# Kernel tuning notes

Measured on AMD Instinct MI355X. Metric: run time of the kernel, lower is better.

The kernel has to match this reference:

```python
import jax, jax.numpy as jnp
import numpy as np

B, T, E, H = 8, 1024, 1024, 16
D = E // H  # head_dim = 64
MAX_OFFSET = 0.5


def setup_inputs() -> dict:
    key = jax.random.key(0)
    ks = jax.random.split(key, 12)
    s = 0.02
    return {
        "query": jax.random.normal(ks[0], (B, T, E), jnp.float32),
        "key_": jax.random.normal(ks[1], (B, T, E), jnp.float32),
        "value": jax.random.normal(ks[2], (B, T, E), jnp.float32),
        "Wq": jax.random.normal(ks[3], (E, E), jnp.float32) * s,
        "bq": jnp.zeros((E,), jnp.float32),
        "Wk": jax.random.normal(ks[4], (E, E), jnp.float32) * s,
        "bk": jnp.zeros((E,), jnp.float32),
        "Wv": jax.random.normal(ks[5], (E, E), jnp.float32) * s,
        "bv": jnp.zeros((E,), jnp.float32),
        "Wo": jax.random.normal(ks[6], (E, E), jnp.float32) * s,
        "bo": jnp.zeros((E,), jnp.float32),
        "bias_table": jax.random.normal(ks[7], (2 * T - 1, H), jnp.float32) * s,
        "offset": jax.random.normal(ks[8], (1,), jnp.float32) * 0.1,
    }


def _temporal_bias(bias_table, offset):
    # relative position index: [T, T] in [0, 2T-2]
    coords = jnp.arange(T)
    rel = (coords[:, None] - coords[None, :]) + (T - 1)
    bounded = jnp.tanh(offset) * MAX_OFFSET  # scalar (shape (1,))
    adj = jnp.clip(rel.astype(jnp.float32) + bounded, 0.0, 2.0 * T - 2.0)
    lo = jnp.floor(adj).astype(jnp.int32)
    hi = jnp.ceil(adj).astype(jnp.int32)
    w = adj - lo.astype(jnp.float32)  # [T, T]
    lo_val = bias_table[lo]  # [T, T, H]
    hi_val = bias_table[hi]  # [T, T, H]
    bias = lo_val * (1.0 - w[..., None]) + hi_val * w[..., None]
    # -> [1, H, T, T]
    return jnp.transpose(bias, (2, 0, 1))[None]


def reference(query, key_, value, Wq, bq, Wk, bk, Wv, bv, Wo, bo, bias_table, offset):
    scale = D ** -0.5
    # torch Linear: x @ W.T + b
    q = (jnp.einsum('bte,fe->btf', query, Wq) + bq).reshape(B, T, H, D).transpose(0, 2, 1, 3)
    k = (jnp.einsum('bte,fe->btf', key_, Wk) + bk).reshape(B, T, H, D).transpose(0, 2, 1, 3)
    v = (jnp.einsum('bte,fe->btf', value, Wv) + bv).reshape(B, T, H, D).transpose(0, 2, 1, 3)
    scores = jnp.einsum('bhqd,bhkd->bhqk', q, k) * scale  # [B, H, T, T]
    scores = scores + _temporal_bias(bias_table, offset)
    attn = jax.nn.softmax(scores, axis=-1)
    out = jnp.einsum('bhqk,bhkd->bhqd', attn, v)  # [B, H, T, D]
    out = out.transpose(0, 2, 1, 3).reshape(B, T, E)
    return jnp.einsum('bte,fe->btf', out, Wo) + bo
```

## Files before the change

### kernel.cpp

```cpp
#include <hip/hip_runtime.h>
#include <hip/hip_bf16.h>
#include <stdint.h>

#define B_ 8
#define T_ 1024
#define E_ 1024
#define H_ 16
#define D_ 64
#define NREL 2047

using bf16 = __hip_bfloat16;
typedef __attribute__((ext_vector_type(8))) short bhalf8;
typedef __attribute__((ext_vector_type(4))) float f32x4;

typedef __attribute__((address_space(3))) uint32_t lds32_t;
typedef const __attribute__((address_space(1))) uint32_t glb32_t;
__device__ __forceinline__ void gld_lds16(const bf16* g, bf16* l) {
  __builtin_amdgcn_global_load_lds((glb32_t*)(const void*)g, (lds32_t*)(void*)l, 16, 0, 0);
}

__global__ __launch_bounds__(256) void cvt_f32_bf16(const float* __restrict__ s,
                                                    bf16* __restrict__ d, int n) {
  const int i = (blockIdx.x * 256 + threadIdx.x) * 8;
  if (i >= n) return;
  const float4 a = *(const float4*)(s + i);
  const float4 b = *(const float4*)(s + i + 4);
  bf16 t[8];
  t[0] = __float2bfloat16(a.x); t[1] = __float2bfloat16(a.y);
  t[2] = __float2bfloat16(a.z); t[3] = __float2bfloat16(a.w);
  t[4] = __float2bfloat16(b.x); t[5] = __float2bfloat16(b.y);
  t[6] = __float2bfloat16(b.z); t[7] = __float2bfloat16(b.w);
  *(bhalf8*)(d + i) = *(const bhalf8*)t;
}

__global__ void bias_pre(const float* __restrict__ table, const float* __restrict__ offset,
                         float* __restrict__ db) {
  const int idx = blockIdx.x * 256 + threadIdx.x;
  if (idx >= NREL * H_) return;
  const int r = idx >> 4;
  const int h = idx & 15;
  const float bounded = tanhf(offset[0]) * 0.5f;
  float adj = (float)r + bounded;
  adj = fminf(fmaxf(adj, 0.f), 2046.f);
  const int lo = (int)floorf(adj);
  const int hi = (int)ceilf(adj);
  const float wgt = adj - (float)lo;
  const float v = table[lo * H_ + h] * (1.f - wgt) + table[hi * H_ + h] * wgt;
  db[h * NREL + r] = v * 1.4426950408889634f;
}

__global__ __launch_bounds__(256, 3) void gemm_qkv(const float* __restrict__ Xq,
                                                   const float* __restrict__ Xk,
                                                   const float* __restrict__ Xv,
                                                   const bf16* __restrict__ Wc,
                                                   const float* __restrict__ bqp,
                                                   const float* __restrict__ bkp,
                                                   const float* __restrict__ bvp,
                                                   bf16* __restrict__ dst) {
  __shared__ bf16 As[128 * 32];
  __shared__ bf16 Bs[128 * 32];
  const int tid = threadIdx.x;
  const int lane = tid & 63;
  const int w = tid >> 6;
  const int quad = lane >> 4;
  const int l15 = lane & 15;
  const int m0 = blockIdx.x * 128;
  const int n0 = blockIdx.y * 128;
  const int z = blockIdx.z;
  const float* A = (z == 0) ? Xq : ((z == 1) ? Xk : Xv);
  const float* bias = (z == 0) ? bqp : ((z == 1) ? bkp : bvp);
  const bf16* W = Wc + (size_t)z * E_ * E_;
  bf16* out = dst + (size_t)z * B_ * T_ * D_ * H_;
  const int wm = (w >> 1) * 64;
  const int wn = (w & 1) * 64;

  const f32x4 zero4 = {0.f, 0.f, 0.f, 0.f};
  f32x4 acc[4][4];
#pragma unroll
  for (int i = 0; i < 4; ++i)
#pragma unroll
    for (int j = 0; j < 4; ++j) acc[i][j] = zero4;

  const int srow = w * 32 + (lane >> 2);
  const int scol = (lane & 3) * 8;
  const float* Ag = A + (size_t)(m0 + srow) * E_ + scol;
  const bf16* Wg = W + (size_t)(n0 + srow) * E_ + scol;
  bf16* As0 = As + w * 1024 + lane * 8;
  bf16* Bs0 = Bs + w * 1024 + lane * 8;

  float4 p0 = *(const float4*)(Ag);
  float4 p1 = *(const float4*)(Ag + 4);
  float4 p2 = *(const float4*)(Ag + (size_t)16 * E_);
  float4 p3 = *(const float4*)(Ag + (size_t)16 * E_ + 4);

  for (int kt = 0; kt < 32; ++kt) {
    __syncthreads();
    const int kc = kt * 32;
    gld_lds16(Wg + kc, Bs0);
    gld_lds16(Wg + (size_t)16 * E_ + kc, Bs0 + 512);
    const float4 a0 = p0, a1 = p1, a2 = p2, a3 = p3;
    if (kt < 31) {
      const int kc2 = kc + 32;
      p0 = *(const float4*)(Ag + kc2);
      p1 = *(const float4*)(Ag + kc2 + 4);
      p2 = *(const float4*)(Ag + (size_t)16 * E_ + kc2);
      p3 = *(const float4*)(Ag + (size_t)16 * E_ + kc2 + 4);
    }
    bf16 t[8];
    t[0] = __float2bfloat16(a0.x); t[1] = __float2bfloat16(a0.y);
    t[2] = __float2bfloat16(a0.z); t[3] = __float2bfloat16(a0.w);
    t[4] = __float2bfloat16(a1.x); t[5] = __float2bfloat16(a1.y);
    t[6] = __float2bfloat16(a1.z); t[7] = __float2bfloat16(a1.w);
    *(bhalf8*)As0 = *(const bhalf8*)t;
    t[0] = __float2bfloat16(a2.x); t[1] = __float2bfloat16(a2.y);
    t[2] = __float2bfloat16(a2.z); t[3] = __float2bfloat16(a2.w);
    t[4] = __float2bfloat16(a3.x); t[5] = __float2bfloat16(a3.y);
    t[6] = __float2bfloat16(a3.z); t[7] = __float2bfloat16(a3.w);
    *(bhalf8*)(As0 + 512) = *(const bhalf8*)t;
    __syncthreads();

    bhalf8 af[4], bfr[4];
#pragma unroll
    for (int t2 = 0; t2 < 4; ++t2) {
      af[t2] = *(const bhalf8*)(As + (wm + t2 * 16 + l15) * 32 + quad * 8);
      bfr[t2] = *(const bhalf8*)(Bs + (wn + t2 * 16 + l15) * 32 + quad * 8);
    }
#pragma unroll
    for (int mt = 0; mt < 4; ++mt)
#pragma unroll
      for (int nt = 0; nt < 4; ++nt)
        acc[mt][nt] = __builtin_amdgcn_mfma_f32_16x16x32_bf16(af[mt], bfr[nt], acc[mt][nt], 0, 0, 0);
  }

#pragma unroll
  for (int mt = 0; mt < 4; ++mt) {
#pragma unroll
    for (int nt = 0; nt < 4; ++nt) {
      const int n = n0 + wn + nt * 16 + l15;
      const float bv = bias[n];
#pragma unroll
      for (int r = 0; r < 4; ++r) {
        const int m = m0 + wm + mt * 16 + quad * 4 + r;
        const float v = acc[mt][nt][r] + bv;
        const int bb = m >> 10, tq = m & 1023, hh = n >> 6, d = n & 63;
        out[(((size_t)bb * H_ + hh) * T_ + tq) * D_ + d] = __float2bfloat16(v);
      }
    }
  }
}

template <int SCATTER, int F32OUT>
__global__ __launch_bounds__(256) void gemm_bt(const bf16* __restrict__ A,
                                               const bf16* __restrict__ W,
                                               const float* __restrict__ bias,
                                               void* __restrict__ dst_) {
  __shared__ bf16 As[128 * 32];
  __shared__ bf16 Bs[128 * 32];
  const int tid = threadIdx.x;
  const int lane = tid & 63;
  const int w = tid >> 6;
  const int quad = lane >> 4;
  const int l15 = lane & 15;
  const int m0 = blockIdx.x * 128;
  const int n0 = blockIdx.y * 128;
  const int wm = (w >> 1) * 64;
  const int wn = (w & 1) * 64;

  const f32x4 zero4 = {0.f, 0.f, 0.f, 0.f};
  f32x4 acc[4][4];
#pragma unroll
  for (int i = 0; i < 4; ++i)
#pragma unroll
    for (int j = 0; j < 4; ++j) acc[i][j] = zero4;

  const int srow0 = w * 32 + (lane >> 2);
  const int scol = (lane & 3) * 8;
  const bf16* Ag = A + (size_t)(m0 + srow0) * E_ + scol;
  const bf16* Wg = W + (size_t)(n0 + srow0) * E_ + scol;
  bf16* As0 = As + w * 1024 + lane * 8;
  bf16* Bs0 = Bs + w * 1024 + lane * 8;

  for (int kt = 0; kt < 32; ++kt) {
    __syncthreads();
    const int kc = kt * 32;
    gld_lds16(Ag + kc, As0);
    gld_lds16(Ag + (size_t)16 * E_ + kc, As0 + 512);
    gld_lds16(Wg + kc, Bs0);
    gld_lds16(Wg + (size_t)16 * E_ + kc, Bs0 + 512);
    __syncthreads();

    bhalf8 af[4], bfr[4];
#pragma unroll
    for (int t = 0; t < 4; ++t) {
      af[t] = *(const bhalf8*)(As + (wm + t * 16 + l15) * 32 + quad * 8);
      bfr[t] = *(const bhalf8*)(Bs + (wn + t * 16 + l15) * 32 + quad * 8);
    }
#pragma unroll
    for (int mt = 0; mt < 4; ++mt)
#pragma unroll
      for (int nt = 0; nt < 4; ++nt)
        acc[mt][nt] = __builtin_amdgcn_mfma_f32_16x16x32_bf16(af[mt], bfr[nt], acc[mt][nt], 0, 0, 0);
  }

#pragma unroll
  for (int mt = 0; mt < 4; ++mt) {
#pragma unroll
    for (int nt = 0; nt < 4; ++nt) {
      const int n = n0 + wn + nt * 16 + l15;
      const float bv = bias[n];
#pragma unroll
      for (int r = 0; r < 4; ++r) {
        const int m = m0 + wm + mt * 16 + quad * 4 + r;
        const float v = acc[mt][nt][r] + bv;
        if (SCATTER) {
          const int bb = m >> 10, t = m & 1023, hh = n >> 6, d = n & 63;
          ((bf16*)dst_)[(((size_t)bb * H_ + hh) * T_ + t) * D_ + d] = __float2bfloat16(v);
        } else if (F32OUT) {
          ((float*)dst_)[(size_t)m * E_ + n] = v;
        } else {
          ((bf16*)dst_)[(size_t)m * E_ + n] = __float2bfloat16(v);
        }
      }
    }
  }
}

__device__ __forceinline__ int ps_off(int row, int colbyte) {
  return row * 128 + (colbyte ^ ((row & 7) << 4));
}

__global__ __launch_bounds__(256, 4) void attn_kernel(const bf16* __restrict__ Q,
                                                      const bf16* __restrict__ K,
                                                      const bf16* __restrict__ V,
                                                      const float* __restrict__ db,
                                                      bf16* __restrict__ xout) {
  const int tid = threadIdx.x;
  const int lane = tid & 63;
  const int w = tid >> 6;
  const int quad = lane >> 4;
  const int l15 = lane & 15;
  const int bh = blockIdx.x;
  const int h = bh & 15;
  const int b = bh >> 4;
  const int q0 = blockIdx.y * 128;

  __shared__ bf16 Vt[64][72];
  __shared__ __align__(16) bf16 Ps[4][32 * 64];
  __shared__ float dbs[1152];

  const size_t base = (size_t)bh * T_ * D_;
  const bf16* Qp = Q + base;
  const bf16* Kp = K + base;
  const bf16* Vp = V + base;
  const float* dbh = db + h * NREL;

  for (int t = tid; t < 1151; t += 256) dbs[t] = dbh[q0 + t];

  const int qw = q0 + w * 32;
  bhalf8 aq[2][2];
#pragma unroll
  for (int mt = 0; mt < 2; ++mt)
#pragma unroll
    for (int ks = 0; ks < 2; ++ks)
      aq[mt][ks] = *(const bhalf8*)(Qp + (size_t)(qw + mt * 16 + l15) * D_ + ks * 32 + quad * 8);

  const f32x4 zero4 = {0.f, 0.f, 0.f, 0.f};
  f32x4 o[2][4];
#pragma unroll
  for (int mt = 0; mt < 2; ++mt)
#pragma unroll
    for (int nt = 0; nt < 4; ++nt) o[mt][nt] = zero4;
  float mrow[2] = {-1e30f, -1e30f};
  float lrow[2] = {0.f, 0.f};

  const int vrow0 = tid >> 3;
  const int vc8 = (tid & 7) * 8;
  bhalf8 vreg[2];
  vreg[0] = *(const bhalf8*)(Vp + (size_t)vrow0 * D_ + vc8);
  vreg[1] = *(const bhalf8*)(Vp + (size_t)(vrow0 + 32) * D_ + vc8);

  char* const psw = (char*)&Ps[w][0];

  for (int it = 0; it < 16; ++it) {
    const int kb = it * 64;
    bhalf8 bk[4][2];
#pragma unroll
    for (int nt = 0; nt < 4; ++nt) {
      const bf16* kr = Kp + (size_t)(kb + nt * 16 + l15) * D_ + quad * 8;
      bk[nt][0] = *(const bhalf8*)kr;
      bk[nt][1] = *(const bhalf8*)(kr + 32);
    }

    __syncthreads();
#pragma unroll
    for (int s = 0; s < 2; ++s) {
      const int row = vrow0 + s * 32;
      const bf16* vp = (const bf16*)&vreg[s];
      const int kvp = (row + vc8) & 63;
#pragma unroll
      for (int j = 0; j < 8; ++j) Vt[vc8 + j][kvp] = vp[j];
    }
    __syncthreads();
    if (it < 15) {
      const int kb2 = kb + 64;
      vreg[0] = *(const bhalf8*)(Vp + (size_t)(kb2 + vrow0) * D_ + vc8);
      vreg[1] = *(const bhalf8*)(Vp + (size_t)(kb2 + vrow0 + 32) * D_ + vc8);
    }

    f32x4 s4[2][4];
    __builtin_amdgcn_s_setprio(1);
#pragma unroll
    for (int nt = 0; nt < 4; ++nt) {
#pragma unroll
      for (int mt = 0; mt < 2; ++mt) {
        f32x4 a = zero4;
        a = __builtin_amdgcn_mfma_f32_16x16x32_bf16(bk[nt][0], aq[mt][0], a, 0, 0, 0);
        a = __builtin_amdgcn_mfma_f32_16x16x32_bf16(bk[nt][1], aq[mt][1], a, 0, 0, 0);
        s4[mt][nt] = a;
      }
    }
    __builtin_amdgcn_s_setprio(0);

#pragma unroll
    for (int mt = 0; mt < 2; ++mt) {
      const int ib = w * 32 + mt * 16 + l15 + 1023 - kb;
      float mnt[4];
#pragma unroll
      for (int nt = 0; nt < 4; ++nt) {
#pragma unroll
        for (int r = 0; r < 4; ++r) {
          const float sv = s4[mt][nt][r] * 0.18033688011112042f + dbs[ib - nt * 16 - quad * 4 - r];
          s4[mt][nt][r] = sv;
        }
        mnt[nt] = fmaxf(fmaxf(s4[mt][nt][0], s4[mt][nt][1]),
                        fmaxf(s4[mt][nt][2], s4[mt][nt][3]));
      }
      float tmx = fmaxf(fmaxf(mnt[0], mnt[1]), fmaxf(mnt[2], mnt[3]));
      tmx = fmaxf(tmx, __shfl_xor(tmx, 16, 64));
      tmx = fmaxf(tmx, __shfl_xor(tmx, 32, 64));
      if (!__all(tmx - mrow[mt] <= 11.0f)) {
        const float mnew = fmaxf(mrow[mt], tmx);
        const float alpha = __builtin_amdgcn_exp2f(mrow[mt] - mnew);
        mrow[mt] = mnew;
        lrow[mt] *= alpha;
#pragma unroll
        for (int nt = 0; nt < 4; ++nt) o[mt][nt] *= alpha;
      }
      const float mcur = mrow[mt];
      float psum[4];
#pragma unroll
      for (int nt = 0; nt < 4; ++nt) {
        float p0 = __builtin_amdgcn_exp2f(s4[mt][nt][0] - mcur);
        float p1 = __builtin_amdgcn_exp2f(s4[mt][nt][1] - mcur);
        float p2 = __builtin_amdgcn_exp2f(s4[mt][nt][2] - mcur);
        float p3 = __builtin_amdgcn_exp2f(s4[mt][nt][3] - mcur);
        s4[mt][nt][0] = p0; s4[mt][nt][1] = p1;
        s4[mt][nt][2] = p2; s4[mt][nt][3] = p3;
        psum[nt] = (p0 + p1) + (p2 + p3);
      }
      float sum = (psum[0] + psum[1]) + (psum[2] + psum[3]);
      sum += __shfl_xor(sum, 16, 64);
      sum += __shfl_xor(sum, 32, 64);
      lrow[mt] += sum;

#pragma unroll
      for (int nt = 0; nt < 4; ++nt) {
        alignas(8) bf16 t4[4];
#pragma unroll
        for (int r = 0; r < 4; ++r) t4[r] = __float2bfloat16(s4[mt][nt][r]);
        *(uint2*)(psw + ps_off(mt * 16 + l15, nt * 32 + quad * 8)) = *(const uint2*)t4;
      }
    }

    bhalf8 pb[2][2];
#pragma unroll
    for (int mt = 0; mt < 2; ++mt)
#pragma unroll
      for (int ks = 0; ks < 2; ++ks)
        pb[mt][ks] = *(const bhalf8*)(psw + ps_off(mt * 16 + l15, ks * 64 + quad * 16));
    const int rot = (l15 >> 3);
    __builtin_amdgcn_s_setprio(1);
#pragma unroll
    for (int nt = 0; nt < 4; ++nt) {
      const int drow = nt * 16 + l15;
#pragma unroll
      for (int ks = 0; ks < 2; ++ks) {
        const int gp = (4 * ks + quad + 2 * nt + rot) & 7;
        const bhalf8 vb = *(const bhalf8*)&Vt[drow][gp * 8];
#pragma unroll
        for (int mt = 0; mt < 2; ++mt)
          o[mt][nt] = __builtin_amdgcn_mfma_f32_16x16x32_bf16(vb, pb[mt][ks], o[mt][nt], 0, 0, 0);
      }
    }
    __builtin_amdgcn_s_setprio(0);
  }

#pragma unroll
  for (int mt = 0; mt < 2; ++mt) {
    const float inv = 1.f / lrow[mt];
#pragma unroll
    for (int nt = 0; nt < 4; ++nt) {
      alignas(8) bf16 t4[4];
#pragma unroll
      for (int r = 0; r < 4; ++r) t4[r] = __float2bfloat16(o[mt][nt][r] * inv);
      *(uint2*)(psw + ps_off(mt * 16 + l15, nt * 32 + quad * 8)) = *(const uint2*)t4;
    }
  }
#pragma unroll
  for (int t = 0; t < 4; ++t) {
    const int idx = t * 64 + lane;
    const int row = idx >> 3;
    const int c = idx & 7;
    const bhalf8 val = *(const bhalf8*)(psw + ps_off(row, c * 16));
    *(bhalf8*)&xout[((size_t)b * T_ + qw + row) * E_ + h * D_ + c * 8] = val;
  }
}

extern "C" void kernel_launch(void* const* d_in, const int* in_sizes, int n_in,
                              void* d_out, int out_size, void* d_ws, size_t ws_size,
                              hipStream_t stream) {
  const float* query = (const float*)d_in[0];
  const float* key_  = (const float*)d_in[1];
  const float* value = (const float*)d_in[2];
  const float* Wq = (const float*)d_in[3];
  const float* bq = (const float*)d_in[4];
  const float* Wk = (const float*)d_in[5];
  const float* bk = (const float*)d_in[6];
  const float* Wv = (const float*)d_in[7];
  const float* bv = (const float*)d_in[8];
  const float* Wo = (const float*)d_in[9];
  const float* bo = (const float*)d_in[10];
  const float* table = (const float*)d_in[11];
  const float* offset = (const float*)d_in[12];
  float* out = (float*)d_out;

  char* ws = (char*)d_ws;
  const size_t ME = (size_t)B_ * T_ * E_;
  const size_t EE = (size_t)E_ * E_;
  float* db = (float*)ws;
  bf16* wc  = (bf16*)(ws + 131072);
  bf16* qb  = wc + 4 * EE;
  bf16* kb  = qb + ME;
  bf16* vb2 = kb + ME;
  bf16* x2  = vb2 + ME;

  dim3 bb(256, 1, 1);
  const int gEE = (int)(EE / 8 / 256);

  bias_pre<<<dim3(128), bb, 0, stream>>>(table, offset, db);

  cvt_f32_bf16<<<dim3(gEE), bb, 0, stream>>>(Wq, wc + 0 * EE, (int)EE);
  cvt_f32_bf16<<<dim3(gEE), bb, 0, stream>>>(Wk, wc + 1 * EE, (int)EE);
  cvt_f32_bf16<<<dim3(gEE), bb, 0, stream>>>(Wv, wc + 2 * EE, (int)EE);
  cvt_f32_bf16<<<dim3(gEE), bb, 0, stream>>>(Wo, wc + 3 * EE, (int)EE);

  gemm_qkv<<<dim3(64, 8, 3), bb, 0, stream>>>(query, key_, value, wc, bq, bk, bv, qb);

  attn_kernel<<<dim3(128, 8, 1), bb, 0, stream>>>(qb, kb, vb2, db, x2);

  gemm_bt<0, 1><<<dim3(64, 8, 1), bb, 0, stream>>>(x2, wc + 3 * EE, bo, out);
}
```

Measured before the change: 354.8 us.

## Double-buffer LDS tiles in projection GEMMs and merge weight conversion launches

Both the QKV projection GEMM and the output GEMM now use two LDS buffers per operand. The next K-tile is loaded, and for QKV the fp32 activations are converted into the alternate buffer, while MFMAs run on the current one. This cuts the loop to one barrier per iteration instead of two and hides global-load latency. The four weight-conversion launches are also merged into one 2D-grid launch. The cost is doubled LDS per block (32 KB), which may lower occupancy, notably against the launch bound of 3 blocks requested for gemm_qkv.

```diff
diff --git a/kernel.cpp b/kernel.cpp
--- a/kernel.cpp
+++ b/kernel.cpp
@@ -19,18 +19,26 @@
   __builtin_amdgcn_global_load_lds((glb32_t*)(const void*)g, (lds32_t*)(void*)l, 16, 0, 0);
 }
 
-__global__ __launch_bounds__(256) void cvt_f32_bf16(const float* __restrict__ s,
-                                                    bf16* __restrict__ d, int n) {
-  const int i = (blockIdx.x * 256 + threadIdx.x) * 8;
-  if (i >= n) return;
-  const float4 a = *(const float4*)(s + i);
-  const float4 b = *(const float4*)(s + i + 4);
+__device__ __forceinline__ bhalf8 cvt8(const float4 a, const float4 b) {
   bf16 t[8];
   t[0] = __float2bfloat16(a.x); t[1] = __float2bfloat16(a.y);
   t[2] = __float2bfloat16(a.z); t[3] = __float2bfloat16(a.w);
   t[4] = __float2bfloat16(b.x); t[5] = __float2bfloat16(b.y);
   t[6] = __float2bfloat16(b.z); t[7] = __float2bfloat16(b.w);
-  *(bhalf8*)(d + i) = *(const bhalf8*)t;
+  return *(const bhalf8*)t;
+}
+
+__global__ __launch_bounds__(256) void cvt_w4(const float* __restrict__ Wq,
+                                              const float* __restrict__ Wk,
+                                              const float* __restrict__ Wv,
+                                              const float* __restrict__ Wo,
+                                              bf16* __restrict__ d) {
+  const int z = blockIdx.y;
+  const float* s = (z == 0) ? Wq : (z == 1) ? Wk : (z == 2) ? Wv : Wo;
+  const int i = (blockIdx.x * 256 + threadIdx.x) * 8;
+  const float4 a = *(const float4*)(s + i);
+  const float4 b = *(const float4*)(s + i + 4);
+  *(bhalf8*)(d + (size_t)z * E_ * E_ + i) = cvt8(a, b);
 }
 
 __global__ void bias_pre(const float* __restrict__ table, const float* __restrict__ offset,
@@ -57,8 +65,8 @@
                                                    const float* __restrict__ bkp,
                                                    const float* __restrict__ bvp,
                                                    bf16* __restrict__ dst) {
-  __shared__ bf16 As[128 * 32];
-  __shared__ bf16 Bs[128 * 32];
+  __shared__ bf16 As[2 * 128 * 32];
+  __shared__ bf16 Bs[2 * 128 * 32];
   const int tid = threadIdx.x;
   const int lane = tid & 63;
   const int w = tid >> 6;
@@ -85,51 +93,51 @@
   const int scol = (lane & 3) * 8;
   const float* Ag = A + (size_t)(m0 + srow) * E_ + scol;
   const bf16* Wg = W + (size_t)(n0 + srow) * E_ + scol;
-  bf16* As0 = As + w * 1024 + lane * 8;
-  bf16* Bs0 = Bs + w * 1024 + lane * 8;
+  const int sidx = w * 1024 + lane * 8;
 
   float4 p0 = *(const float4*)(Ag);
   float4 p1 = *(const float4*)(Ag + 4);
   float4 p2 = *(const float4*)(Ag + (size_t)16 * E_);
   float4 p3 = *(const float4*)(Ag + (size_t)16 * E_ + 4);
+  *(bhalf8*)(As + sidx) = cvt8(p0, p1);
+  *(bhalf8*)(As + sidx + 512) = cvt8(p2, p3);
+  gld_lds16(Wg, Bs + sidx);
+  gld_lds16(Wg + (size_t)16 * E_, Bs + sidx + 512);
+  p0 = *(const float4*)(Ag + 32);
+  p1 = *(const float4*)(Ag + 36);
+  p2 = *(const float4*)(Ag + (size_t)16 * E_ + 32);
+  p3 = *(const float4*)(Ag + (size_t)16 * E_ + 36);
+  __syncthreads();
 
   for (int kt = 0; kt < 32; ++kt) {
-    __syncthreads();
-    const int kc = kt * 32;
-    gld_lds16(Wg + kc, Bs0);
-    gld_lds16(Wg + (size_t)16 * E_ + kc, Bs0 + 512);
-    const float4 a0 = p0, a1 = p1, a2 = p2, a3 = p3;
+    const int cur = (kt & 1) * 4096;
+    bhalf8 af[4], bfr[4];
+#pragma unroll
+    for (int t2 = 0; t2 < 4; ++t2) {
+      af[t2] = *(const bhalf8*)(As + cur + (wm + t2 * 16 + l15) * 32 + quad * 8);
+      bfr[t2] = *(const bhalf8*)(Bs + cur + (wn + t2 * 16 + l15) * 32 + quad * 8);
+    }
     if (kt < 31) {
-      const int kc2 = kc + 32;
-      p0 = *(const float4*)(Ag + kc2);
-      p1 = *(const float4*)(Ag + kc2 + 4);
-      p2 = *(const float4*)(Ag + (size_t)16 * E_ + kc2);
-      p3 = *(const float4*)(Ag + (size_t)16 * E_ + kc2 + 4);
-    }
-    bf16 t[8];
-    t[0] = __float2bfloat16(a0.x); t[1] = __float2bfloat16(a0.y);
-    t[2] = __float2bfloat16(a0.z); t[3] = __float2bfloat16(a0.w);
-    t[4] = __float2bfloat16(a1.x); t[5] = __float2bfloat16(a1.y);
-    t[6] = __float2bfloat16(a1.z); t[7] = __float2bfloat16(a1.w);
-    *(bhalf8*)As0 = *(const bhalf8*)t;
-    t[0] = __float2bfloat16(a2.x); t[1] = __float2bfloat16(a2.y);
-    t[2] = __float2bfloat16(a2.z); t[3] = __float2bfloat16(a2.w);
-    t[4] = __float2bfloat16(a3.x); t[5] = __float2bfloat16(a3.y);
-    t[6] = __float2bfloat16(a3.z); t[7] = __float2bfloat16(a3.w);
-    *(bhalf8*)(As0 + 512) = *(const bhalf8*)t;
-    __syncthreads();
-
-    bhalf8 af[4], bfr[4];
-#pragma unroll
-    for (int t2 = 0; t2 < 4; ++t2) {
-      af[t2] = *(const bhalf8*)(As + (wm + t2 * 16 + l15) * 32 + quad * 8);
-      bfr[t2] = *(const bhalf8*)(Bs + (wn + t2 * 16 + l15) * 32 + quad * 8);
+      const int nxt = 4096 - cur;
+      const int kc = (kt + 1) * 32;
+      gld_lds16(Wg + kc, Bs + nxt + sidx);
+      gld_lds16(Wg + (size_t)16 * E_ + kc, Bs + nxt + sidx + 512);
+      *(bhalf8*)(As + nxt + sidx) = cvt8(p0, p1);
+      *(bhalf8*)(As + nxt + sidx + 512) = cvt8(p2, p3);
+      if (kt < 30) {
+        const int kc2 = kc + 32;
+        p0 = *(const float4*)(Ag + kc2);
+        p1 = *(const float4*)(Ag + kc2 + 4);
+        p2 = *(const float4*)(Ag + (size_t)16 * E_ + kc2);
+        p3 = *(const float4*)(Ag + (size_t)16 * E_ + kc2 + 4);
+      }
     }
 #pragma unroll
     for (int mt = 0; mt < 4; ++mt)
 #pragma unroll
       for (int nt = 0; nt < 4; ++nt)
         acc[mt][nt] = __builtin_amdgcn_mfma_f32_16x16x32_bf16(af[mt], bfr[nt], acc[mt][nt], 0, 0, 0);
+    __syncthreads();
   }
 
 #pragma unroll
@@ -154,8 +162,8 @@
                                                const bf16* __restrict__ W,
                                                const float* __restrict__ bias,
                                                void* __restrict__ dst_) {
-  __shared__ bf16 As[128 * 32];
-  __shared__ bf16 Bs[128 * 32];
+  __shared__ bf16 As[2 * 128 * 32];
+  __shared__ bf16 Bs[2 * 128 * 32];
   const int tid = threadIdx.x;
   const int lane = tid & 63;
   const int w = tid >> 6;
@@ -177,29 +185,36 @@
   const int scol = (lane & 3) * 8;
   const bf16* Ag = A + (size_t)(m0 + srow0) * E_ + scol;
   const bf16* Wg = W + (size_t)(n0 + srow0) * E_ + scol;
-  bf16* As0 = As + w * 1024 + lane * 8;
-  bf16* Bs0 = Bs + w * 1024 + lane * 8;
+  const int sidx = w * 1024 + lane * 8;
+
+  gld_lds16(Ag, As + sidx);
+  gld_lds16(Ag + (size_t)16 * E_, As + sidx + 512);
+  gld_lds16(Wg, Bs + sidx);
+  gld_lds16(Wg + (size_t)16 * E_, Bs + sidx + 512);
+  __syncthreads();
 
   for (int kt = 0; kt < 32; ++kt) {
-    __syncthreads();
-    const int kc = kt * 32;
-    gld_lds16(Ag + kc, As0);
-    gld_lds16(Ag + (size_t)16 * E_ + kc, As0 + 512);
-    gld_lds16(Wg + kc, Bs0);
-    gld_lds16(Wg + (size_t)16 * E_ + kc, Bs0 + 512);
-    __syncthreads();
-
+    const int cur = (kt & 1) * 4096;
     bhalf8 af[4], bfr[4];
 #pragma unroll
     for (int t = 0; t < 4; ++t) {
-      af[t] = *(const bhalf8*)(As + (wm + t * 16 + l15) * 32 + quad * 8);
-      bfr[t] = *(const bhalf8*)(Bs + (wn + t * 16 + l15) * 32 + quad * 8);
+      af[t] = *(const bhalf8*)(As + cur + (wm + t * 16 + l15) * 32 + quad * 8);
+      bfr[t] = *(const bhalf8*)(Bs + cur + (wn + t * 16 + l15) * 32 + quad * 8);
+    }
+    if (kt < 31) {
+      const int nxt = 4096 - cur;
+      const int kc = (kt + 1) * 32;
+      gld_lds16(Ag + kc, As + nxt + sidx);
+      gld_lds16(Ag + (size_t)16 * E_ + kc, As + nxt + sidx + 512);
+      gld_lds16(Wg + kc, Bs + nxt + sidx);
+      gld_lds16(Wg + (size_t)16 * E_ + kc, Bs + nxt + sidx + 512);
     }
 #pragma unroll
     for (int mt = 0; mt < 4; ++mt)
 #pragma unroll
       for (int nt = 0; nt < 4; ++nt)
         acc[mt][nt] = __builtin_amdgcn_mfma_f32_16x16x32_bf16(af[mt], bfr[nt], acc[mt][nt], 0, 0, 0);
+    __syncthreads();
   }
 
 #pragma unroll
@@ -448,11 +463,7 @@
   const int gEE = (int)(EE / 8 / 256);
 
   bias_pre<<<dim3(128), bb, 0, stream>>>(table, offset, db);
-
-  cvt_f32_bf16<<<dim3(gEE), bb, 0, stream>>>(Wq, wc + 0 * EE, (int)EE);
-  cvt_f32_bf16<<<dim3(gEE), bb, 0, stream>>>(Wk, wc + 1 * EE, (int)EE);
-  cvt_f32_bf16<<<dim3(gEE), bb, 0, stream>>>(Wv, wc + 2 * EE, (int)EE);
-  cvt_f32_bf16<<<dim3(gEE), bb, 0, stream>>>(Wo, wc + 3 * EE, (int)EE);
+  cvt_w4<<<dim3(gEE, 4), bb, 0, stream>>>(Wq, Wk, Wv, Wo, wc);
 
   gemm_qkv<<<dim3(64, 8, 3), bb, 0, stream>>>(query, key_, value, wc, bq, bk, bv, qb);
 
```

Measured after the change: 346.8 us. 2.2% less time.
